# Kernel tuning notes

Hardware: AMD Instinct MI355X
Metric: run time of the kernel (lower is better)

Reference implementation:

```python
import jax, jax.numpy as jnp
import numpy as np


def _grid_neighbors(H, W):
    # 4-neighbor grid adjacency for the Mesh([H, W]) graph
    idx = np.arange(H * W).reshape(H, W)
    p = np.full((H + 2, W + 2), -1, dtype=np.int64)
    p[1:-1, 1:-1] = idx
    nbrs = np.stack([p[0:H, 1:W + 1], p[2:H + 2, 1:W + 1], p[1:H + 1, 0:W], p[1:H + 1, 2:W + 2]], axis=-1).reshape(H * W, 4)
    mask = (nbrs >= 0).astype(np.float32)
    return np.where(nbrs >= 0, nbrs, 0), mask, mask.sum(-1) + 1.0


def _conv(x, w, b):
    y = jax.lax.conv_general_dilated(x, w, (1, 1), 'SAME', dimension_numbers=('NCHW', 'OIHW', 'NCHW'))
    return y + b[None, :, None, None]


def _dconv(x, w1, b1, w2, b2):
    return jax.nn.relu(_conv(jax.nn.relu(_conv(x, w1, b1)), w2, b2))


def _maxpool(x):
    return jax.lax.reduce_window(x, -jnp.inf, jax.lax.max, (1, 1, 2, 2), (1, 1, 2, 2), 'VALID')


def _convT(x, w, b):
    # kernel=2, stride=2 transposed conv (non-overlapping upsample)
    y = jax.lax.conv_transpose(x, w, (2, 2), 'VALID', dimension_numbers=('NCHW', 'HWIO', 'NCHW'))
    return y + b[None, :, None, None]


def _gconv(X, W, b, nbrs, mask, deg):
    # mesh graph conv: D^-1 (A + I) X W, irregular gather over grid adjacency
    g = X[:, nbrs, :]                                          # [B, N, 4, C]
    agg = ((g * mask[None, :, :, None]).sum(2) + X) / deg[None, :, None]
    return jax.nn.relu(jnp.einsum('bnc,cd->bnd', agg, W) + b[None, None, :])


def _forward(x, d1w1, d1b1, d1w2, d1b2, d2w1, d2b1, d2w2, d2b2, md1w, md1b, md2w, md2b, mbw, mbb, mu1w, mu1b, mu2w, mu2b, u3tw, u3tb, u3w1, u3b1, u3w2, u3b2, u4tw, u4tb, u4w1, u4b1, u4w2, u4b2, ow, ob):
    b1 = _dconv(x, d1w1, d1b1, d1w2, d1b2)                     # [1,64,256,256]
    b2 = _dconv(_maxpool(b1), d2w1, d2b1, d2w2, d2b2)          # [1,128,128,128]
    fe = _maxpool(b2)                                           # [1,128,64,64]
    fe = jnp.pad(fe, ((0, 0), (0, 0), (1, 1), (1, 1)))          # pad -> 66x66
    B, C, Hm, Wm = fe.shape
    nbrs, mask, deg = _grid_neighbors(Hm, Wm)
    nbrs, mask, deg = jnp.asarray(nbrs), jnp.asarray(mask), jnp.asarray(deg)
    X = fe.reshape(B, C, Hm * Wm).transpose(0, 2, 1)            # [1, 4356, 128]
    bp1 = _gconv(X, md1w, md1b, nbrs, mask, deg)                # 256 (skip)
    bp2 = _gconv(bp1, md2w, md2b, nbrs, mask, deg)              # 512 (skip)
    Xb = _gconv(bp2, mbw, mbb, nbrs, mask, deg)                 # 1024 mesh bottleneck
    X = _gconv(Xb, mu1w, mu1b, nbrs, mask, deg) + bp2           # 512
    X = _gconv(X, mu2w, mu2b, nbrs, mask, deg) + bp1            # 256
    fe = X.transpose(0, 2, 1).reshape(B, 256, Hm, Wm)[:, :, 1:-1, 1:-1]  # unpad -> 64x64
    u3 = _convT(fe, u3tw, u3tb)                                 # [1,128,128,128]
    fe = _dconv(jnp.concatenate([b2, u3], 1), u3w1, u3b1, u3w2, u3b2)
    u4 = _convT(fe, u4tw, u4tb)                                 # [1,64,256,256]
    fe = _dconv(jnp.concatenate([b1, u4], 1), u4w1, u4b1, u4w2, u4b2)
    return _conv(fe, ow, ob)[:, 0]                              # [1,256,256]


def setup_inputs():
    ks = iter(jax.random.split(jax.random.key(0), 40))
    def W(shape, fan_in):
        return jax.random.normal(next(ks), shape, jnp.float32) * np.float32(np.sqrt(2.0 / fan_in))
    def Z(n):
        return jnp.zeros((n,), jnp.float32)
    return {
        'x': jax.random.normal(next(ks), (1, 3, 256, 256), jnp.float32),
        'd1w1': W((64, 3, 3, 3), 27), 'd1b1': Z(64), 'd1w2': W((64, 64, 3, 3), 576), 'd1b2': Z(64),
        'd2w1': W((128, 64, 3, 3), 576), 'd2b1': Z(128), 'd2w2': W((128, 128, 3, 3), 1152), 'd2b2': Z(128),
        'md1w': W((128, 256), 128), 'md1b': Z(256),
        'md2w': W((256, 512), 256), 'md2b': Z(512),
        'mbw': W((512, 1024), 512), 'mbb': Z(1024),
        'mu1w': W((1024, 512), 1024), 'mu1b': Z(512),
        'mu2w': W((512, 256), 512), 'mu2b': Z(256),
        'u3tw': W((2, 2, 256, 128), 1024), 'u3tb': Z(128),
        'u3w1': W((128, 256, 3, 3), 2304), 'u3b1': Z(128), 'u3w2': W((128, 128, 3, 3), 1152), 'u3b2': Z(128),
        'u4tw': W((2, 2, 128, 64), 512), 'u4tb': Z(64),
        'u4w1': W((64, 128, 3, 3), 1152), 'u4b1': Z(64), 'u4w2': W((64, 64, 3, 3), 576), 'u4b2': Z(64),
        'ow': W((1, 64, 3, 3), 576), 'ob': Z(1),
    }


def reference(x, d1w1, d1b1, d1w2, d1b2, d2w1, d2b1, d2w2, d2b2, md1w, md1b, md2w, md2b, mbw, mbb, mu1w, mu1b, mu2w, mu2b, u3tw, u3tb, u3w1, u3b1, u3w2, u3b2, u4tw, u4tb, u4w1, u4b1, u4w2, u4b2, ow, ob):
    return _forward(x, d1w1, d1b1, d1w2, d1b2, d2w1, d2b1, d2w2, d2b2, md1w, md1b, md2w, md2b, mbw, mbb, mu1w, mu1b, mu2w, mu2b, u3tw, u3tb, u3w1, u3b1, u3w2, u3b2, u4tw, u4tb, u4w1, u4b1, u4w2, u4b2, ow, ob)
```

## Files before the change

kernel.cpp:

```cpp
#include <hip/hip_runtime.h>
#include <cstddef>

#define TPB 256

typedef __attribute__((ext_vector_type(8))) short short8;
typedef __attribute__((ext_vector_type(4))) float f32x4;

__device__ inline unsigned short f2bf(float f) {
    unsigned int u = __builtin_bit_cast(unsigned int, f);
    u += 0x7fffu + ((u >> 16) & 1u);
    return (unsigned short)(u >> 16);
}
__device__ inline float bf2f(unsigned short h) {
    unsigned int u = ((unsigned int)h) << 16;
    return __builtin_bit_cast(float, u);
}

struct TapOffs { int o[9]; };

template<int CHUNKS>
__global__ __launch_bounds__(TPB) void k_conv3n(
    const unsigned short* __restrict__ A0, const unsigned short* __restrict__ Wf,
    const float* __restrict__ bias, unsigned short* __restrict__ O0,
    int AP, int tilesX, int OMS, int OP, int NTtot)
{
    constexpr int Cs  = CHUNKS * 64;
    constexpr int KC2 = CHUNKS * 2;

    int lane = threadIdx.x & 63, wave = threadIdx.x >> 6;
    int ml = lane & 15, kq = lane >> 4;
    int nb = blockIdx.y;
    int tileX = blockIdx.x % tilesX, gy = blockIdx.x / tilesX;
    int gx0 = tileX * 64 + wave * 16;

    const unsigned short* Abase = A0 + (size_t)(gy - 1) * AP
                                     + (size_t)(gx0 + ml - 1) * Cs + kq * 8;
    const unsigned short* Bp = Wf + (size_t)(nb * 4) * 512 + lane * 8;

    f32x4 acc[4];
    #pragma unroll
    for (int nt = 0; nt < 4; ++nt) acc[nt] = (f32x4){0.f, 0.f, 0.f, 0.f};

    #pragma unroll
    for (int tap = 0; tap < 9; ++tap) {
        int ky = tap / 3, kx = tap - (tap / 3) * 3;
        const unsigned short* Ar = Abase + (size_t)ky * AP + kx * Cs;
        const unsigned short* Bt = Bp + (size_t)(tap * KC2) * NTtot * 512;
        #pragma unroll
        for (int q = 0; q < KC2; ++q) {
            short8 b[4];
            #pragma unroll
            for (int nt = 0; nt < 4; ++nt)
                b[nt] = *(const short8*)(Bt + ((size_t)q * NTtot + nt) * 512);
            short8 a = *(const short8*)(Ar + q * 32);
            #pragma unroll
            for (int nt = 0; nt < 4; ++nt)
                acc[nt] = __builtin_amdgcn_mfma_f32_16x16x32_bf16(a, b[nt], acc[nt], 0, 0, 0);
        }
    }

    unsigned short* Orow = O0 + (size_t)gy * OP + (size_t)nb * 64;
    int gx = gx0 + kq * 4;
    #pragma unroll
    for (int nt = 0; nt < 4; ++nt) {
        float bv = bias[nb * 64 + nt * 16 + ml];
        #pragma unroll
        for (int r = 0; r < 4; ++r) {
            float v = fmaxf(acc[nt][r] + bv, 0.f);
            Orow[(size_t)(gx + r) * OMS + nt * 16 + ml] = f2bf(v);
        }
    }
}

template<int KCW>
__global__ __launch_bounds__(TPB) void k_gemmS(
    const unsigned short* __restrict__ A0, const unsigned short* __restrict__ Wf,
    const float* __restrict__ bias, const unsigned short* __restrict__ resid,
    unsigned short* __restrict__ O0, int NTtot,
    int AP, int Wimg, int OMS, int OP, int relu, int ct, int ctDy, int ctDx)
{
    constexpr int K = KCW * 128;
    __shared__ float red[12 * 4 * 64 * 4];
    int lane = threadIdx.x & 63, wave = threadIdx.x >> 6;
    int ml = lane & 15, kq = lane >> 4;
    int m0 = blockIdx.x * 64, nb = blockIdx.y;

    const unsigned short* Wb = Wf;
    unsigned short* Ob = O0;
    if (ct) {
        int tp = blockIdx.z;
        Wb += (size_t)(tp * KCW * 4) * NTtot * 512;
        int dy = 1 - (tp >> 1), dx = 1 - (tp & 1);
        Ob += (size_t)dy * ctDy + (size_t)dx * ctDx;
    }

    const unsigned short* Ap[4];
    #pragma unroll
    for (int i = 0; i < 4; ++i) {
        int mf = (wave + i) & 3;
        int m = m0 + mf * 16;
        int y = m / Wimg, x = m - y * Wimg;
        Ap[i] = A0 + (size_t)y * AP + (size_t)(x + ml) * K + wave * (KCW * 32) + kq * 8;
    }
    const unsigned short* Bp = Wb + ((size_t)(wave * KCW) * NTtot + nb * 4) * 512 + lane * 8;

    f32x4 acc[4][4];
    #pragma unroll
    for (int i = 0; i < 4; ++i)
        #pragma unroll
        for (int nt = 0; nt < 4; ++nt) acc[i][nt] = (f32x4){0.f, 0.f, 0.f, 0.f};

    #pragma unroll
    for (int q = 0; q < KCW; ++q) {
        short8 b[4];
        #pragma unroll
        for (int nt = 0; nt < 4; ++nt)
            b[nt] = *(const short8*)(Bp + ((size_t)q * NTtot + nt) * 512);
        short8 a[4];
        #pragma unroll
        for (int i = 0; i < 4; ++i)
            a[i] = *(const short8*)(Ap[i] + q * 32);
        #pragma unroll
        for (int i = 0; i < 4; ++i)
            #pragma unroll
            for (int nt = 0; nt < 4; ++nt)
                acc[i][nt] = __builtin_amdgcn_mfma_f32_16x16x32_bf16(a[i], b[nt], acc[i][nt], 0, 0, 0);
    }

    #pragma unroll
    for (int i = 1; i < 4; ++i) {
        int s = wave * 3 + (i - 1);
        #pragma unroll
        for (int nt = 0; nt < 4; ++nt)
            *(f32x4*)&red[(((s * 4 + nt) * 64) + lane) * 4] = acc[i][nt];
    }
    __syncthreads();
    #pragma unroll
    for (int w2 = 0; w2 < 4; ++w2) {
        if (w2 == wave) continue;
        int i = (wave - w2) & 3;
        int s = w2 * 3 + (i - 1);
        #pragma unroll
        for (int nt = 0; nt < 4; ++nt) {
            f32x4 v = *(const f32x4*)&red[(((s * 4 + nt) * 64) + lane) * 4];
            acc[0][nt] += v;
        }
    }

    int mrow = m0 + wave * 16 + kq * 4;
    int y = mrow / Wimg, x = mrow - y * Wimg;
    unsigned short* Ot = Ob + (size_t)y * OP + (size_t)x * OMS + nb * 64;
    const unsigned short* Rt = resid ? resid + (size_t)mrow * OMS + nb * 64 : nullptr;
    #pragma unroll
    for (int nt = 0; nt < 4; ++nt) {
        float bv = bias[nb * 64 + nt * 16 + ml];
        #pragma unroll
        for (int r = 0; r < 4; ++r) {
            float v = acc[0][nt][r] + bv;
            if (relu) v = fmaxf(v, 0.f);
            if (Rt) v += bf2f(Rt[(size_t)r * OMS + nt * 16 + ml]);
            Ot[(size_t)r * OMS + nt * 16 + ml] = f2bf(v);
        }
    }
}

template<int KC>
__global__ __launch_bounds__(TPB) void k_gemmN(
    const unsigned short* __restrict__ A0, const unsigned short* __restrict__ Wf,
    const float* __restrict__ bias, unsigned short* __restrict__ O0,
    int Cs, int AP, int Wimg, int OMS, int OP, int NTtot, int relu,
    int ct, int ctDy, int ctDx)
{
    int lane = threadIdx.x & 63, wave = threadIdx.x >> 6;
    int ml = lane & 15, kq = lane >> 4;
    int nb = blockIdx.y;

    const unsigned short* Wb = Wf;
    unsigned short* Ob = O0;
    if (ct) {
        int tp = blockIdx.z;
        Wb += (size_t)(tp * KC) * NTtot * 512;
        int dy = 1 - (tp >> 1), dx = 1 - (tp & 1);
        Ob += (size_t)dy * ctDy + (size_t)dx * ctDx;
    }
    int m0 = blockIdx.x * 64 + wave * 16;
    int y = m0 / Wimg, x = m0 - y * Wimg;
    const unsigned short* Arow = A0 + (size_t)y * AP + (size_t)(x + ml) * Cs + kq * 8;
    const unsigned short* Bp = Wb + (size_t)(nb * 4) * 512 + lane * 8;

    f32x4 acc[4];
    #pragma unroll
    for (int nt = 0; nt < 4; ++nt) acc[nt] = (f32x4){0.f, 0.f, 0.f, 0.f};

    #pragma unroll
    for (int q = 0; q < KC; ++q) {
        short8 b[4];
        #pragma unroll
        for (int nt = 0; nt < 4; ++nt)
            b[nt] = *(const short8*)(Bp + ((size_t)q * NTtot + nt) * 512);
        short8 a = *(const short8*)(Arow + q * 32);
        #pragma unroll
        for (int nt = 0; nt < 4; ++nt)
            acc[nt] = __builtin_amdgcn_mfma_f32_16x16x32_bf16(a, b[nt], acc[nt], 0, 0, 0);
    }

    unsigned short* Ot = Ob + (size_t)y * OP + (size_t)(x + kq * 4) * OMS + (size_t)nb * 64;
    #pragma unroll
    for (int nt = 0; nt < 4; ++nt) {
        float bv = bias[nb * 64 + nt * 16 + ml];
        #pragma unroll
        for (int r = 0; r < 4; ++r) {
            float v = acc[nt][r] + bv;
            if (relu) v = fmaxf(v, 0.f);
            Ot[(size_t)r * OMS + nt * 16 + ml] = f2bf(v);
        }
    }
}

template<int MW, int KC>
__global__ __launch_bounds__(TPB) void k_gemm(
    const unsigned short* __restrict__ A0, const unsigned short* __restrict__ Wf,
    const float* __restrict__ bias, unsigned short* __restrict__ O0,
    int Cs, int AP, int Wimg, int OMS, int OP,
    int T, TapOffs toffs, int NTtot, int relu)
{
    int lane = threadIdx.x & 63, wave = threadIdx.x >> 6;
    int ml = lane & 15, kq = lane >> 4;
    int nb = blockIdx.y;
    const unsigned short* WbB = Wf + (size_t)(nb * 4) * 512 + lane * 8;

    int fy[MW], fx[MW];
    const unsigned short* Af[MW];
    #pragma unroll
    for (int f = 0; f < MW; ++f) {
        int mf = (blockIdx.x * 4 + wave) * (16 * MW) + f * 16;
        int y = mf / Wimg, x = mf - y * Wimg;
        fy[f] = y; fx[f] = x;
        Af[f] = A0 + (size_t)y * AP + (size_t)(x + ml) * Cs + kq * 8;
    }

    f32x4 acc[MW][4];
    #pragma unroll
    for (int f = 0; f < MW; ++f)
        #pragma unroll
        for (int nt = 0; nt < 4; ++nt) acc[f][nt] = (f32x4){0.f, 0.f, 0.f, 0.f};

    for (int tp = 0; tp < T; ++tp) {
        int toff = toffs.o[tp];
        const unsigned short* Wt = WbB + (size_t)(tp * KC) * NTtot * 512;
        #pragma unroll
        for (int q = 0; q < KC; ++q) {
            short8 b[4];
            #pragma unroll
            for (int nt = 0; nt < 4; ++nt)
                b[nt] = *(const short8*)(Wt + (size_t)q * NTtot * 512 + nt * 512);
            short8 a[MW];
            #pragma unroll
            for (int f = 0; f < MW; ++f)
                a[f] = *(const short8*)(Af[f] + toff + q * 32);
            #pragma unroll
            for (int f = 0; f < MW; ++f)
                #pragma unroll
                for (int nt = 0; nt < 4; ++nt)
                    acc[f][nt] = __builtin_amdgcn_mfma_f32_16x16x32_bf16(a[f], b[nt], acc[f][nt], 0, 0, 0);
        }
    }

    #pragma unroll
    for (int f = 0; f < MW; ++f) {
        unsigned short* Ot = O0 + (size_t)fy[f] * OP + (size_t)(fx[f] + kq * 4) * OMS + (size_t)nb * 64;
        #pragma unroll
        for (int nt = 0; nt < 4; ++nt) {
            float bv = bias[nb * 64 + nt * 16 + ml];
            #pragma unroll
            for (int r = 0; r < 4; ++r) {
                float v = acc[f][nt][r] + bv;
                if (relu) v = fmaxf(v, 0.f);
                Ot[(size_t)r * OMS + nt * 16 + ml] = f2bf(v);
            }
        }
    }
}

struct PackArgs {
    const float* w[15];
    int cum[16];
    int mode[15], KC[15], NT[15], K[15], N[15];
};
__global__ __launch_bounds__(TPB) void k_pack_all(
    PackArgs pa, unsigned short* __restrict__ dst, int total)
{
    int idx = blockIdx.x * TPB + threadIdx.x;
    if (idx >= total) return;
    int e = 0;
    #pragma unroll
    for (int i = 1; i < 15; ++i) e += (idx >= pa.cum[i]);
    int local = idx - pa.cum[e];
    const float* w = pa.w[e];
    int KC = pa.KC[e], NT = pa.NT[e], K = pa.K[e], N = pa.N[e], mode = pa.mode[e];

    int j = local & 7, l = (local >> 3) & 63;
    int r = local >> 9;
    int ntg = r % NT; int r2 = r / NT;
    int q = r2 % KC; int tp = r2 / KC;
    int k = q * 32 + (l >> 4) * 8 + j;
    int n = ntg * 16 + (l & 15);
    float v = 0.f;
    if (mode == 0) { int ky = tp / 3, kx = tp % 3; v = w[(size_t)(n * K + k) * 9 + ky * 3 + kx]; }
    else if (mode == 1) { v = w[(size_t)k * N + n]; }
    else if (mode == 2) { v = w[((size_t)tp * K + k) * N + n]; }
    else { if (k < 27) { int tap = k / 3, c = k % 3; int ky = tap / 3, kx = tap % 3;
                         v = w[((n * 3 + c) * 3 + ky) * 3 + kx]; } }
    dst[idx] = f2bf(v);
}

struct ZArgs { int off[10]; int cum[11]; int W2[10]; int H2[10]; int Cs[10]; };
__global__ __launch_bounds__(TPB) void k_zero_all(
    ZArgs za, unsigned short* __restrict__ W, int total)
{
    int idx = blockIdx.x * TPB + threadIdx.x;
    if (idx >= total) return;
    int e = 0;
    #pragma unroll
    for (int i = 1; i < 10; ++i) e += (idx >= za.cum[i]);
    int local = idx - za.cum[e];
    int W2 = za.W2[e], H2 = za.H2[e], Cs = za.Cs[e];
    int topbot = 2 * W2 * Cs;
    int iy, ix, c;
    if (local < topbot) {
        int row = local / (W2 * Cs); int rest = local - row * (W2 * Cs);
        iy = row ? (H2 - 1) : 0; ix = rest / Cs; c = rest - (rest / Cs) * Cs;
    } else {
        int idx2 = local - topbot;
        int per = (H2 - 2) * Cs;
        int side = idx2 / per; int rest = idx2 - side * per;
        iy = 1 + rest / Cs; ix = side ? (W2 - 1) : 0; c = rest - (rest / Cs) * Cs;
    }
    W[(size_t)za.off[e] + ((size_t)iy * W2 + ix) * Cs + c] = 0;
}

__global__ __launch_bounds__(TPB) void k_im2col(
    const float* __restrict__ x, unsigned short* __restrict__ xcol)
{
    int idx = blockIdx.x * TPB + threadIdx.x;
    if (idx >= 65536 * 32) return;
    int k = idx & 31, m = idx >> 5;
    int y = m >> 8, xx = m & 255;
    float v = 0.f;
    if (k < 27) {
        int tap = k / 3, c = k - tap * 3;
        int ty = tap / 3, tx = tap % 3;
        int yy = y + ty - 1, xp = xx + tx - 1;
        if (yy >= 0 && yy < 256 && xp >= 0 && xp < 256)
            v = x[c * 65536 + yy * 256 + xp];
    }
    xcol[idx] = f2bf(v);
}

__global__ __launch_bounds__(TPB) void k_maxpool(
    const unsigned short* __restrict__ inI, unsigned short* __restrict__ outI,
    int Wo, int C4, int CsIn, int inPitch, int CsOut, int outPitch, int total)
{
    int idx = blockIdx.x * TPB + threadIdx.x;
    if (idx >= total) return;
    int c4 = idx % C4; int p = idx / C4;
    int x = p % Wo, y = p / Wo;
    const unsigned short* ip = inI + (size_t)(2 * y) * inPitch + (size_t)(2 * x) * CsIn + c4 * 4;
    ushort4 a = *(const ushort4*)(ip);
    ushort4 b = *(const ushort4*)(ip + CsIn);
    ushort4 c = *(const ushort4*)(ip + inPitch);
    ushort4 d = *(const ushort4*)(ip + inPitch + CsIn);
    ushort4 o;
    o.x = f2bf(fmaxf(fmaxf(bf2f(a.x), bf2f(b.x)), fmaxf(bf2f(c.x), bf2f(d.x))));
    o.y = f2bf(fmaxf(fmaxf(bf2f(a.y), bf2f(b.y)), fmaxf(bf2f(c.y), bf2f(d.y))));
    o.z = f2bf(fmaxf(fmaxf(bf2f(a.z), bf2f(b.z)), fmaxf(bf2f(c.z), bf2f(d.z))));
    o.w = f2bf(fmaxf(fmaxf(bf2f(a.w), bf2f(b.w)), fmaxf(bf2f(c.w), bf2f(d.w))));
    *(ushort4*)(outI + (size_t)y * outPitch + (size_t)x * CsOut + c4 * 4) = o;
}

__global__ __launch_bounds__(TPB) void k_gagg(
    const unsigned short* __restrict__ X, unsigned short* __restrict__ agg,
    int C, int total)
{
    int idx = blockIdx.x * TPB + threadIdx.x;
    if (idx >= total) return;
    int C4 = C >> 2;
    int c4 = idx % C4; int n = idx / C4;
    int i = n / 66, j = n - i * 66;
    size_t base = (size_t)n * C + c4 * 4;
    ushort4 s = *(const ushort4*)(X + base);
    float v0 = bf2f(s.x), v1 = bf2f(s.y), v2 = bf2f(s.z), v3 = bf2f(s.w);
    float cnt = 1.f;
    if (i > 0)  { ushort4 u = *(const ushort4*)(X + base - (size_t)66 * C);
                  v0 += bf2f(u.x); v1 += bf2f(u.y); v2 += bf2f(u.z); v3 += bf2f(u.w); cnt += 1.f; }
    if (i < 65) { ushort4 u = *(const ushort4*)(X + base + (size_t)66 * C);
                  v0 += bf2f(u.x); v1 += bf2f(u.y); v2 += bf2f(u.z); v3 += bf2f(u.w); cnt += 1.f; }
    if (j > 0)  { ushort4 u = *(const ushort4*)(X + base - C);
                  v0 += bf2f(u.x); v1 += bf2f(u.y); v2 += bf2f(u.z); v3 += bf2f(u.w); cnt += 1.f; }
    if (j < 65) { ushort4 u = *(const ushort4*)(X + base + C);
                  v0 += bf2f(u.x); v1 += bf2f(u.y); v2 += bf2f(u.z); v3 += bf2f(u.w); cnt += 1.f; }
    float inv = 1.f / cnt;
    ushort4 o;
    o.x = f2bf(v0 * inv); o.y = f2bf(v1 * inv); o.z = f2bf(v2 * inv); o.w = f2bf(v3 * inv);
    *(ushort4*)(agg + base) = o;
}

__global__ __launch_bounds__(TPB) void k_outconv(
    const unsigned short* __restrict__ vI, const float* __restrict__ ow,
    const float* __restrict__ ob, float* __restrict__ out)
{
    __shared__ float wl[576];
    for (int i = threadIdx.x; i < 576; i += TPB) wl[i] = ow[i];
    __syncthreads();
    int p = blockIdx.x * TPB + threadIdx.x;
    int y = p >> 8, x = p & 255;
    float acc = ob[0];
    #pragma unroll
    for (int ky = 0; ky < 3; ++ky)
        #pragma unroll
        for (int kx = 0; kx < 3; ++kx) {
            const unsigned short* ip = vI + (size_t)((y + ky - 1) * 258 + (x + kx - 1)) * 64;
            int wb = ky * 3 + kx;
            for (int c = 0; c < 64; c += 4) {
                ushort4 uv = *(const ushort4*)(ip + c);
                acc += bf2f(uv.x) * wl[c * 9 + wb] + bf2f(uv.y) * wl[(c + 1) * 9 + wb]
                     + bf2f(uv.z) * wl[(c + 2) * 9 + wb] + bf2f(uv.w) * wl[(c + 3) * 9 + wb];
            }
        }
    out[p] = acc;
}

static inline TapOffs zero_toffs() { TapOffs t = {}; return t; }

extern "C" void kernel_launch(void* const* d_in, const int* in_sizes, int n_in,
                              void* d_out, int out_size, void* d_ws, size_t ws_size,
                              hipStream_t stream) {
    const float* x    = (const float*)d_in[0];
    const float* d1w1 = (const float*)d_in[1];  const float* d1b1 = (const float*)d_in[2];
    const float* d1w2 = (const float*)d_in[3];  const float* d1b2 = (const float*)d_in[4];
    const float* d2w1 = (const float*)d_in[5];  const float* d2b1 = (const float*)d_in[6];
    const float* d2w2 = (const float*)d_in[7];  const float* d2b2 = (const float*)d_in[8];
    const float* md1w = (const float*)d_in[9];  const float* md1b = (const float*)d_in[10];
    const float* md2w = (const float*)d_in[11]; const float* md2b = (const float*)d_in[12];
    const float* mbw  = (const float*)d_in[13]; const float* mbb  = (const float*)d_in[14];
    const float* mu1w = (const float*)d_in[15]; const float* mu1b = (const float*)d_in[16];
    const float* mu2w = (const float*)d_in[17]; const float* mu2b = (const float*)d_in[18];
    const float* u3tw = (const float*)d_in[19]; const float* u3tb = (const float*)d_in[20];
    const float* u3w1 = (const float*)d_in[21]; const float* u3b1 = (const float*)d_in[22];
    const float* u3w2 = (const float*)d_in[23]; const float* u3b2 = (const float*)d_in[24];
    const float* u4tw = (const float*)d_in[25]; const float* u4tb = (const float*)d_in[26];
    const float* u4w1 = (const float*)d_in[27]; const float* u4b1 = (const float*)d_in[28];
    const float* u4w2 = (const float*)d_in[29]; const float* u4b2 = (const float*)d_in[30];
    const float* ow   = (const float*)d_in[31]; const float* ob   = (const float*)d_in[32];
    float* out = (float*)d_out;

    unsigned short* W = (unsigned short*)d_ws;

    const size_t XCOL = 0;
    const size_t A1   = 2097152;
    const size_t CAT4 = 6357248;
    const size_t P1   = 14877440;
    const size_t T2   = 15959040;
    const size_t CAT3 = 18122240;
    const size_t X0   = 22448640;
    const size_t BP1  = 23006208;
    const size_t BP2  = 24185856;
    const size_t XB   = 26545152;
    const size_t XC   = 31263744;
    const size_t XD   = 33623040;
    const size_t V3A  = 34802688;
    const size_t V3B  = 36965888;
    const size_t V4A  = 39129088;
    const size_t V4B  = 43389184;
    const size_t AGG  = 47649280;
    const size_t WP   = 52367872;

    const size_t a1I   = A1 + 259 * 64;
    const size_t cat4I = CAT4 + 259 * 128;
    const size_t p1I   = P1 + 131 * 64;
    const size_t t2I   = T2 + 131 * 128;
    const size_t cat3I = CAT3 + 131 * 256;
    const size_t X0I   = X0 + 67 * 128;
    const size_t XdI   = XD + 67 * 256;
    const size_t v3aI  = V3A + 131 * 128;
    const size_t v3bI  = V3B + 131 * 128;
    const size_t v4aI  = V4A + 259 * 64;
    const size_t v4bI  = V4B + 259 * 64;

    dim3 blk(TPB);
    const int BIG = 1 << 28;

    {
        ZArgs za;
        const int off[10] = {(int)A1,(int)CAT4,(int)P1,(int)T2,(int)CAT3,(int)V3A,(int)V3B,(int)V4A,(int)V4B,(int)X0};
        const int w2 [10] = {258,258,130,130,130,130,130,258,258,66};
        const int h2 [10] = {258,258,130,130,130,130,130,258,258,66};
        const int cs [10] = {64,128,64,128,256,128,128,64,64,128};
        int cum = 0;
        for (int i = 0; i < 10; ++i) {
            za.off[i]=off[i]; za.W2[i]=w2[i]; za.H2[i]=h2[i]; za.Cs[i]=cs[i];
            za.cum[i]=cum; cum += (w2[i]*h2[i] - (w2[i]-2)*(h2[i]-2))*cs[i];
        }
        za.cum[10]=cum;
        k_zero_all<<<dim3((cum + TPB - 1) / TPB), blk, 0, stream>>>(za, W, cum);
    }

    {
        PackArgs pa;
        const float* ws_[15] = {d1w1,d1w2,d2w1,d2w2,md1w,md2w,mbw,mu1w,mu2w,u3tw,u3w1,u3w2,u4tw,u4w1,u4w2};
        const int mode[15] = {3,0,0,0,1,1,1,1,1,2,0,0,2,0,0};
        const int kc [15] = {1,2,2,4,4,8,16,32,16,8,8,4,4,4,2};
        const int nt [15] = {4,4,8,8,16,32,64,32,16,8,8,8,4,4,4};
        const int kk [15] = {32,64,64,128,128,256,512,1024,512,256,256,128,128,128,64};
        const int nn [15] = {64,64,128,128,256,512,1024,512,256,128,128,128,64,64,64};
        const int tt [15] = {1,9,9,9,1,1,1,1,1,4,9,9,4,9,9};
        int cum = 0;
        for (int i = 0; i < 15; ++i) {
            pa.w[i]=ws_[i]; pa.mode[i]=mode[i]; pa.KC[i]=kc[i]; pa.NT[i]=nt[i];
            pa.K[i]=kk[i]; pa.N[i]=nn[i]; pa.cum[i]=cum;
            cum += tt[i]*kc[i]*nt[i]*512;
        }
        pa.cum[15]=cum;
        k_pack_all<<<dim3((cum + TPB - 1) / TPB), blk, 0, stream>>>(pa, W + WP, cum);
    }
    const size_t pw_d1w1=WP+0, pw_d1w2=WP+2048, pw_d2w1=WP+38912, pw_d2w2=WP+112640,
        pw_md1=WP+260096, pw_md2=WP+292864, pw_mb=WP+423936, pw_mu1=WP+948224,
        pw_mu2=WP+1472512, pw_u3t=WP+1603584, pw_u3w1=WP+1734656, pw_u3w2=WP+2029568,
        pw_u4t=WP+2177024, pw_u4w1=WP+2209792, pw_u4w2=WP+2283520;

    k_im2col<<<dim3(8192), blk, 0, stream>>>(x, W + XCOL);
    k_gemm<2,1><<<dim3(512,1), blk, 0, stream>>>(W + XCOL, W + pw_d1w1, d1b1,
        W + a1I, 32, 8192, 256, 64, 258*64, 1, zero_toffs(), 4, 1);
    k_conv3n<1><<<dim3(1024,1), blk, 0, stream>>>(W + a1I, W + pw_d1w2, d1b2,
        W + cat4I, 258*64, 4, 128, 258*128, 4);
    k_maxpool<<<dim3(1024), blk, 0, stream>>>(W + cat4I, W + p1I, 128, 16, 128, 258*128, 64, 130*64, 128*128*16);
    k_conv3n<1><<<dim3(256,2), blk, 0, stream>>>(W + p1I, W + pw_d2w1, d2b1,
        W + t2I, 130*64, 2, 128, 130*128, 8);
    k_conv3n<2><<<dim3(256,2), blk, 0, stream>>>(W + t2I, W + pw_d2w2, d2b2,
        W + cat3I, 130*128, 2, 256, 130*256, 8);
    k_maxpool<<<dim3(512), blk, 0, stream>>>(W + cat3I, W + X0I, 64, 32, 256, 130*256, 128, 66*128, 64*64*32);

    k_gagg<<<dim3(545), blk, 0, stream>>>(W + X0, W + AGG, 128, 4356*32);
    k_gemmS<1><<<dim3(72,4), blk, 0, stream>>>(W + AGG, W + pw_md1, md1b, nullptr,
        W + BP1, 16, 0, BIG, 256, 0, 1, 0, 0, 0);
    k_gagg<<<dim3(1089), blk, 0, stream>>>(W + BP1, W + AGG, 256, 4356*64);
    k_gemmS<2><<<dim3(72,8), blk, 0, stream>>>(W + AGG, W + pw_md2, md2b, nullptr,
        W + BP2, 32, 0, BIG, 512, 0, 1, 0, 0, 0);
    k_gagg<<<dim3(2178), blk, 0, stream>>>(W + BP2, W + AGG, 512, 4356*128);
    k_gemmS<4><<<dim3(72,16), blk, 0, stream>>>(W + AGG, W + pw_mb, mbb, nullptr,
        W + XB, 64, 0, BIG, 1024, 0, 1, 0, 0, 0);
    k_gagg<<<dim3(4356), blk, 0, stream>>>(W + XB, W + AGG, 1024, 4356*256);
    k_gemmS<8><<<dim3(72,8), blk, 0, stream>>>(W + AGG, W + pw_mu1, mu1b, W + BP2,
        W + XC, 32, 0, BIG, 512, 0, 1, 0, 0, 0);
    k_gagg<<<dim3(2178), blk, 0, stream>>>(W + XC, W + AGG, 512, 4356*128);
    k_gemmS<4><<<dim3(72,4), blk, 0, stream>>>(W + AGG, W + pw_mu2, mu2b, W + BP1,
        W + XD, 16, 0, BIG, 256, 0, 1, 0, 0, 0);

    k_gemmS<2><<<dim3(64,2,4), blk, 0, stream>>>(W + XdI, W + pw_u3t, u3tb, nullptr,
        W + cat3I + 128, 8, 66*256, 64, 512, 2*130*256, 0, 1, 130*256, 256);
    k_conv3n<4><<<dim3(256,2), blk, 0, stream>>>(W + cat3I, W + pw_u3w1, u3b1,
        W + v3aI, 130*256, 2, 128, 130*128, 8);
    k_conv3n<2><<<dim3(256,2), blk, 0, stream>>>(W + v3aI, W + pw_u3w2, u3b2,
        W + v3bI, 130*128, 2, 128, 130*128, 8);

    k_gemmN<4><<<dim3(256,1,4), blk, 0, stream>>>(W + v3bI, W + pw_u4t, u4tb,
        W + cat4I + 64, 128, 130*128, 128, 256, 2*258*128, 4, 0, 1, 258*128, 128);
    k_conv3n<2><<<dim3(1024,1), blk, 0, stream>>>(W + cat4I, W + pw_u4w1, u4b1,
        W + v4aI, 258*128, 4, 64, 258*64, 4);
    k_conv3n<1><<<dim3(1024,1), blk, 0, stream>>>(W + v4aI, W + pw_u4w2, u4b2,
        W + v4bI, 258*64, 4, 64, 258*64, 4);

    k_outconv<<<dim3(256), blk, 0, stream>>>(W + v4bI, ow, ob, out);
}
```

Measured before the change: 430.5 us.

## Stage conv weights in LDS with double buffering and widen M tile per wave

Replaces the 3x3 conv kernel with a version that stages weight fragments into shared memory using async global_load_lds, double-buffered across (channel chunk, ky) groups. Each wave can now compute MW 16-row M fragments, reusing B fragments across them, so the 256x256 convs launch half as many blocks. The aim is to cut redundant global weight loads per wave and raise MFMA density. The cost is 48KB of LDS per block and a barrier per group, which may lower occupancy.

Measured after the change: 390.3 us. -9.3%, faster.

```diff
diff --git a/kernel.cpp b/kernel.cpp
--- a/kernel.cpp
+++ b/kernel.cpp
@@ -18,56 +18,93 @@
 
 struct TapOffs { int o[9]; };
 
-template<int CHUNKS>
-__global__ __launch_bounds__(TPB) void k_conv3n(
+template<int CHUNKS, int MW>
+__global__ __launch_bounds__(TPB) void k_conv3s(
     const unsigned short* __restrict__ A0, const unsigned short* __restrict__ Wf,
     const float* __restrict__ bias, unsigned short* __restrict__ O0,
     int AP, int tilesX, int OMS, int OP, int NTtot)
 {
     constexpr int Cs  = CHUNKS * 64;
     constexpr int KC2 = CHUNKS * 2;
+    __shared__ unsigned short Bs[2][12288];
 
     int lane = threadIdx.x & 63, wave = threadIdx.x >> 6;
     int ml = lane & 15, kq = lane >> 4;
     int nb = blockIdx.y;
     int tileX = blockIdx.x % tilesX, gy = blockIdx.x / tilesX;
-    int gx0 = tileX * 64 + wave * 16;
+    int gx0 = tileX * (MW * 64) + wave * (MW * 16);
 
     const unsigned short* Abase = A0 + (size_t)(gy - 1) * AP
                                      + (size_t)(gx0 + ml - 1) * Cs + kq * 8;
-    const unsigned short* Bp = Wf + (size_t)(nb * 4) * 512 + lane * 8;
-
-    f32x4 acc[4];
-    #pragma unroll
-    for (int nt = 0; nt < 4; ++nt) acc[nt] = (f32x4){0.f, 0.f, 0.f, 0.f};
-
-    #pragma unroll
-    for (int tap = 0; tap < 9; ++tap) {
-        int ky = tap / 3, kx = tap - (tap / 3) * 3;
-        const unsigned short* Ar = Abase + (size_t)ky * AP + kx * Cs;
-        const unsigned short* Bt = Bp + (size_t)(tap * KC2) * NTtot * 512;
-        #pragma unroll
-        for (int q = 0; q < KC2; ++q) {
-            short8 b[4];
+
+    f32x4 acc[MW][4];
+    #pragma unroll
+    for (int mf = 0; mf < MW; ++mf)
+        #pragma unroll
+        for (int nt = 0; nt < 4; ++nt) acc[mf][nt] = (f32x4){0.f, 0.f, 0.f, 0.f};
+
+    const int G = CHUNKS * 3;
+
+    auto stageB = [&](int g) {
+        int ch = g / 3, ky = g - (g / 3) * 3;
+        unsigned short* bd = Bs[g & 1];
+        #pragma unroll
+        for (int it = 0; it < 6; ++it) {
+            int u = threadIdx.x + it * TPB;
+            int e = u * 8;
+            int kxq = e >> 11;
+            int rem = e & 2047;
+            int kx = kxq >> 1, q = kxq & 1;
+            const unsigned short* src = Wf
+                + ((size_t)((ky * 3 + kx) * KC2 + ch * 2 + q) * NTtot + nb * 4) * 512 + rem;
+            unsigned short* dst = &bd[(u & ~63) * 8];
+            __builtin_amdgcn_global_load_lds(
+                (const __attribute__((address_space(1))) unsigned int*)src,
+                (__attribute__((address_space(3))) unsigned int*)dst, 16, 0, 0);
+        }
+    };
+
+    stageB(0);
+    __syncthreads();
+    for (int g = 0; g < G; ++g) {
+        if (g + 1 < G) stageB(g + 1);
+        int ch = g / 3, ky = g - (g / 3) * 3;
+        const unsigned short* Ar = Abase + (size_t)ky * AP + ch * 64;
+        const unsigned short* Bb = &Bs[g & 1][lane * 8];
+        #pragma unroll
+        for (int kx = 0; kx < 3; ++kx) {
             #pragma unroll
-            for (int nt = 0; nt < 4; ++nt)
-                b[nt] = *(const short8*)(Bt + ((size_t)q * NTtot + nt) * 512);
-            short8 a = *(const short8*)(Ar + q * 32);
+            for (int q = 0; q < 2; ++q) {
+                short8 b[4];
+                #pragma unroll
+                for (int nt = 0; nt < 4; ++nt)
+                    b[nt] = *(const short8*)(Bb + (kx * 2 + q) * 2048 + nt * 512);
+                short8 a[MW];
+                #pragma unroll
+                for (int mf = 0; mf < MW; ++mf)
+                    a[mf] = *(const short8*)(Ar + (size_t)(kx + mf * 16) * Cs + q * 32);
+                #pragma unroll
+                for (int mf = 0; mf < MW; ++mf)
+                    #pragma unroll
+                    for (int nt = 0; nt < 4; ++nt)
+                        acc[mf][nt] = __builtin_amdgcn_mfma_f32_16x16x32_bf16(a[mf], b[nt], acc[mf][nt], 0, 0, 0);
+            }
+        }
+        __syncthreads();
+    }
+
+    unsigned short* Orow = O0 + (size_t)gy * OP + (size_t)nb * 64;
+    #pragma unroll
+    for (int mf = 0; mf < MW; ++mf) {
+        int gx = gx0 + mf * 16 + kq * 4;
+        #pragma unroll
+        for (int nt = 0; nt < 4; ++nt) {
+            float bv = bias[nb * 64 + nt * 16 + ml];
             #pragma unroll
-            for (int nt = 0; nt < 4; ++nt)
-                acc[nt] = __builtin_amdgcn_mfma_f32_16x16x32_bf16(a, b[nt], acc[nt], 0, 0, 0);
-        }
-    }
-
-    unsigned short* Orow = O0 + (size_t)gy * OP + (size_t)nb * 64;
-    int gx = gx0 + kq * 4;
-    #pragma unroll
-    for (int nt = 0; nt < 4; ++nt) {
-        float bv = bias[nb * 64 + nt * 16 + ml];
-        #pragma unroll
-        for (int r = 0; r < 4; ++r) {
-            float v = fmaxf(acc[nt][r] + bv, 0.f);
-            Orow[(size_t)(gx + r) * OMS + nt * 16 + ml] = f2bf(v);
+            for (int r = 0; r < 4; ++r) {
+                float v = fmaxf(acc[mf][nt][r] + bv, 0.f);
+                Orow[(size_t)(gx + r) * OMS + nt * 16 + ml] = f2bf(v);
+            }
         }
     }
 }
@@ -531,12 +568,12 @@
     k_im2col<<<dim3(8192), blk, 0, stream>>>(x, W + XCOL);
     k_gemm<2,1><<<dim3(512,1), blk, 0, stream>>>(W + XCOL, W + pw_d1w1, d1b1,
         W + a1I, 32, 8192, 256, 64, 258*64, 1, zero_toffs(), 4, 1);
-    k_conv3n<1><<<dim3(1024,1), blk, 0, stream>>>(W + a1I, W + pw_d1w2, d1b2,
-        W + cat4I, 258*64, 4, 128, 258*128, 4);
+    k_conv3s<1,2><<<dim3(512,1), blk, 0, stream>>>(W + a1I, W + pw_d1w2, d1b2,
+        W + cat4I, 258*64, 2, 128, 258*128, 4);
     k_maxpool<<<dim3(1024), blk, 0, stream>>>(W + cat4I, W + p1I, 128, 16, 128, 258*128, 64, 130*64, 128*128*16);
-    k_conv3n<1><<<dim3(256,2), blk, 0, stream>>>(W + p1I, W + pw_d2w1, d2b1,
+    k_conv3s<1,1><<<dim3(256,2), blk, 0, stream>>>(W + p1I, W + pw_d2w1, d2b1,
         W + t2I, 130*64, 2, 128, 130*128, 8);
-    k_conv3n<2><<<dim3(256,2), blk, 0, stream>>>(W + t2I, W + pw_d2w2, d2b2,
+    k_conv3s<2,1><<<dim3(256,2), blk, 0, stream>>>(W + t2I, W + pw_d2w2, d2b2,
         W + cat3I, 130*128, 2, 256, 130*256, 8);
     k_maxpool<<<dim3(512), blk, 0, stream>>>(W + cat3I, W + X0I, 64, 32, 256, 130*256, 128, 66*128, 64*64*32);
 
@@ -558,17 +595,17 @@
 
     k_gemmS<2><<<dim3(64,2,4), blk, 0, stream>>>(W + XdI, W + pw_u3t, u3tb, nullptr,
         W + cat3I + 128, 8, 66*256, 64, 512, 2*130*256, 0, 1, 130*256, 256);
-    k_conv3n<4><<<dim3(256,2), blk, 0, stream>>>(W + cat3I, W + pw_u3w1, u3b1,
+    k_conv3s<4,1><<<dim3(256,2), blk, 0, stream>>>(W + cat3I, W + pw_u3w1, u3b1,
         W + v3aI, 130*256, 2, 128, 130*128, 8);
-    k_conv3n<2><<<dim3(256,2), blk, 0, stream>>>(W + v3aI, W + pw_u3w2, u3b2,
+    k_conv3s<2,1><<<dim3(256,2), blk, 0, stream>>>(W + v3aI, W + pw_u3w2, u3b2,
         W + v3bI, 130*128, 2, 128, 130*128, 8);
 
     k_gemmN<4><<<dim3(256,1,4), blk, 0, stream>>>(W + v3bI, W + pw_u4t, u4tb,
         W + cat4I + 64, 128, 130*128, 128, 256, 2*258*128, 4, 0, 1, 258*128, 128);
-    k_conv3n<2><<<dim3(1024,1), blk, 0, stream>>>(W + cat4I, W + pw_u4w1, u4b1,
-        W + v4aI, 258*128, 4, 64, 258*64, 4);
-    k_conv3n<1><<<dim3(1024,1), blk, 0, stream>>>(W + v4aI, W + pw_u4w2, u4b2,
-        W + v4bI, 258*64, 4, 64, 258*64, 4);
+    k_conv3s<2,2><<<dim3(512,1), blk, 0, stream>>>(W + cat4I, W + pw_u4w1, u4b1,
+        W + v4aI, 258*128, 2, 64, 258*64, 4);
+    k_conv3s<1,2><<<dim3(512,1), blk, 0, stream>>>(W + v4aI, W + pw_u4w2, u4b2,
+        W + v4bI, 258*64, 2, 64, 258*64, 4);
 
     k_outconv<<<dim3(256), blk, 0, stream>>>(W + v4bI, ow, ob, out);
 }
```
